# Performance work log

Hardware: AMD Instinct MI355X
Metric: run time of the kernel (lower is better)

## Reference

```python
import jax, jax.numpy as jnp
import numpy as np

DECAY_EPS = 1e-8  # matches F.cosine_similarity eps
DECAY_RATE = 0.999  # buffer decay_rate


def setup_inputs() -> dict:
    key = jax.random.key(0)
    ks = jax.random.split(key, 6)
    B, M, D = 256, 65536, 1024
    return {
        "query": jax.random.normal(ks[0], (B, D), dtype=jnp.float32),
        "mem_keys": jax.random.normal(ks[1], (M, D), dtype=jnp.float32),
        "mem_values": jax.random.normal(ks[2], (M, D), dtype=jnp.float32),
        "importance": jax.random.uniform(ks[3], (M,), dtype=jnp.float32),
        "access_times": jax.random.randint(ks[4], (M,), 0, 1000, dtype=jnp.int32),
        "access_counts": jax.random.randint(ks[5], (M,), 1, 50, dtype=jnp.int32),
        "current_time": 1000,
        "top_k": 8,
    }


def reference(query, mem_keys, mem_values, importance, access_times, access_counts, current_time, top_k):
    # Batched version of AdaptiveMemoryBuffer.retrieve.
    # query: [B, D]; mem_keys/mem_values: [M, D]; importance/access_*: [M]
    qn = query / jnp.maximum(jnp.linalg.norm(query, axis=-1, keepdims=True), DECAY_EPS)
    kn = mem_keys / jnp.maximum(jnp.linalg.norm(mem_keys, axis=-1, keepdims=True), DECAY_EPS)
    sim = qn @ kn.T  # [B, M] cosine similarity

    dt = (current_time - access_times).astype(jnp.float32)           # time since access
    retention = jnp.power(jnp.float32(DECAY_RATE), dt)               # forgetting curve
    freq_bonus = jnp.log1p(access_counts.astype(jnp.float32))        # log(1 + count)
    scores = sim * (retention * importance * freq_bonus)[None, :]    # [B, M]

    top_scores, top_idx = jax.lax.top_k(scores, top_k)                # [B, k]
    weights = jax.nn.softmax(top_scores, axis=-1)                     # [B, k]
    combined = jnp.einsum('bk,bkd->bd', weights, mem_values[top_idx]) # weighted gather
    confidence = weights.max(axis=-1)                                 # [B]
    return combined, confidence
```

## Files before the change

kernel.cpp:

```cpp
#include <hip/hip_runtime.h>
#include <math.h>
#include <float.h>

typedef __attribute__((ext_vector_type(8))) short short8;
typedef __attribute__((ext_vector_type(8))) ushort ushort8;
typedef __attribute__((ext_vector_type(4))) float f32x4;

namespace {

constexpr int B = 256;
constexpr int M = 65536;
constexpr int D = 1024;
constexpr float DECAY_EPS = 1e-8f;
constexpr float DECAY_RATE = 0.999f;

constexpr int BN = 64;
constexpr int BK = 32;
constexpr int KSTEPS = D / BK;

constexpr int CHUNKS = 8;
constexpr int CHUNK = M / CHUNKS;
constexpr int NCAND = CHUNKS * 8;

__device__ inline ushort f2bf(float f) {
  union { float f; unsigned u; } v; v.f = f;
  unsigned r = v.u + 0x7fffu + ((v.u >> 16) & 1u);
  return (ushort)(r >> 16);
}

__device__ inline float dot4(float4 a) {
  return a.x * a.x + a.y * a.y + a.z * a.z + a.w * a.w;
}

__global__ void prep_q_kernel(const float* __restrict__ q, ushort* __restrict__ qnf) {
  const int r = blockIdx.x;
  const int t = threadIdx.x;
  float4 v = reinterpret_cast<const float4*>(q + (size_t)r * D)[t];
  float ss = dot4(v);
#pragma unroll
  for (int off = 32; off; off >>= 1) ss += __shfl_down(ss, off, 64);
  __shared__ float red[4];
  if ((t & 63) == 0) red[t >> 6] = ss;
  __syncthreads();
  const float inv = 1.0f / fmaxf(sqrtf(red[0] + red[1] + red[2] + red[3]), DECAY_EPS);
  ushort4 o;
  o.x = f2bf(v.x * inv); o.y = f2bf(v.y * inv);
  o.z = f2bf(v.z * inv); o.w = f2bf(v.w * inv);
  const int k0 = t * 4;
  const int kt = k0 >> 5;
  const int lane_slot = (r & 15) + 16 * ((k0 & 31) >> 3);
  const int j0 = k0 & 7;
  *reinterpret_cast<ushort4*>(qnf + (size_t)(kt * 16 + (r >> 4)) * 512 + lane_slot * 8 + j0) = o;
}

__global__ __launch_bounds__(256) void score_gemm_kernel(
    const ushort* __restrict__ qnf, const float* __restrict__ keys,
    const float* __restrict__ importance, const int* __restrict__ atimes,
    const int* __restrict__ acnts, const int* __restrict__ ctime,
    ushort* __restrict__ scores) {
  __shared__ alignas(16) ushort Bs[2][BN * BK];
  __shared__ float cscale[BN];

  const int t = threadIdx.x;
  const int lane = t & 63;
  const int w = t >> 6;
  const int jb = blockIdx.x * BN;

  const int rw = t >> 2;
  const int cw = t & 3;
  const float* kptr = keys + (size_t)(jb + rw) * D + cw * 8;
  const int woff = rw * BK + ((cw ^ ((rw >> 1) & 3)) * 8);

  f32x4 acc[4][4];
#pragma unroll
  for (int f = 0; f < 4; ++f)
#pragma unroll
    for (int n = 0; n < 4; ++n) acc[f][n] = (f32x4)(0.0f);

  float kn2 = 0.0f;

  {
    float4 v0 = *reinterpret_cast<const float4*>(kptr);
    float4 v1 = *reinterpret_cast<const float4*>(kptr + 4);
    kn2 += dot4(v0) + dot4(v1);
    short8 pk;
    pk[0] = (short)f2bf(v0.x); pk[1] = (short)f2bf(v0.y);
    pk[2] = (short)f2bf(v0.z); pk[3] = (short)f2bf(v0.w);
    pk[4] = (short)f2bf(v1.x); pk[5] = (short)f2bf(v1.y);
    pk[6] = (short)f2bf(v1.z); pk[7] = (short)f2bf(v1.w);
    *reinterpret_cast<short8*>(&Bs[0][woff]) = pk;
  }
  __syncthreads();

  int roff[4];
#pragma unroll
  for (int nf = 0; nf < 4; ++nf) {
    const int row = nf * 16 + (lane & 15);
    roff[nf] = row * BK + (((lane >> 4) ^ ((row >> 1) & 3)) * 8);
  }

  for (int kt = 0; kt < KSTEPS; ++kt) {
    const int cur = kt & 1;
    float4 nv0, nv1;
    if (kt + 1 < KSTEPS) {
      nv0 = *reinterpret_cast<const float4*>(kptr + (kt + 1) * BK);
      nv1 = *reinterpret_cast<const float4*>(kptr + (kt + 1) * BK + 4);
    }
    short8 a[4];
    const short8* ap = reinterpret_cast<const short8*>(qnf) + (size_t)(kt * 16 + w * 4) * 64 + lane;
#pragma unroll
    for (int f = 0; f < 4; ++f) a[f] = ap[f * 64];
    short8 bb[4];
#pragma unroll
    for (int nf = 0; nf < 4; ++nf)
      bb[nf] = *reinterpret_cast<const short8*>(&Bs[cur][roff[nf]]);
#pragma unroll
    for (int f = 0; f < 4; ++f)
#pragma unroll
      for (int nf = 0; nf < 4; ++nf)
        acc[f][nf] = __builtin_amdgcn_mfma_f32_16x16x32_bf16(a[f], bb[nf], acc[f][nf], 0, 0, 0);
    if (kt + 1 < KSTEPS) {
      kn2 += dot4(nv0) + dot4(nv1);
      short8 pk;
      pk[0] = (short)f2bf(nv0.x); pk[1] = (short)f2bf(nv0.y);
      pk[2] = (short)f2bf(nv0.z); pk[3] = (short)f2bf(nv0.w);
      pk[4] = (short)f2bf(nv1.x); pk[5] = (short)f2bf(nv1.y);
      pk[6] = (short)f2bf(nv1.z); pk[7] = (short)f2bf(nv1.w);
      *reinterpret_cast<short8*>(&Bs[cur ^ 1][woff]) = pk;
    }
    __syncthreads();
  }

  kn2 += __shfl_xor(kn2, 1, 64);
  kn2 += __shfl_xor(kn2, 2, 64);
  if (cw == 0) {
    const int j = jb + rw;
    const float dt = (float)(ctime[0] - atimes[j]);
    const float mult = powf(DECAY_RATE, dt) * importance[j] * log1pf((float)acnts[j]);
    cscale[rw] = mult / fmaxf(sqrtf(kn2), DECAY_EPS);
  }
  __syncthreads();

  const int q = lane & 15;
  float cs[4];
#pragma unroll
  for (int nf = 0; nf < 4; ++nf) cs[nf] = cscale[nf * 16 + q];
#pragma unroll
  for (int f = 0; f < 4; ++f) {
    const int row0 = (w * 4 + f) * 16 + ((lane >> 4) << 2);
#pragma unroll
    for (int nf = 0; nf < 4; ++nf) {
#pragma unroll
      for (int rr = 0; rr < 4; ++rr) {
        const float v = acc[f][nf][rr] * cs[nf];
        const float vn = __shfl_xor(v, 1, 64);
        if (!(q & 1)) {
          const uint pk = (uint)f2bf(v) | ((uint)f2bf(vn) << 16);
          *reinterpret_cast<uint*>(
              scores + (size_t)(row0 + rr) * M + jb + nf * 16 + q) = pk;
        }
      }
    }
  }
}

__global__ __launch_bounds__(256) void topk_partial_kernel(
    const ushort* __restrict__ scores, int* __restrict__ cand_i) {
  const int b = blockIdx.y;
  const int c = blockIdx.x;
  const int t = threadIdx.x;
  const int lane = t & 63, w = t >> 6;
  const ushort8* base8 =
      reinterpret_cast<const ushort8*>(scores + (size_t)b * M + (size_t)c * CHUNK);

  uint s8[8];
#pragma unroll
  for (int i = 0; i < 8; ++i) s8[i] = 0;

  auto ins = [&](uint x) {
    if (x > s8[0]) {
#pragma unroll
      for (int i = 0; i < 8; ++i) {
        const bool up = (i < 7) && (x > s8[i + 1]);
        const uint keep = (x > s8[i]) ? x : s8[i];
        s8[i] = up ? s8[i + 1] : keep;
      }
    }
  };

  const uint jbase = (uint)c * CHUNK;
#pragma unroll
  for (int it = 0; it < CHUNK / (256 * 8); ++it) {
    const int slot = it * 256 + t;
    const ushort8 v = base8[slot];
    const uint j0 = jbase + (uint)slot * 8;
#pragma unroll
    for (int e = 0; e < 8; ++e) {
      const ushort s = (ushort)v[e];
      const ushort key = (s & 0x8000) ? (ushort)~s : (ushort)(s | 0x8000);
      ins(((uint)key << 16) | ((j0 + e) & 0xFFFFu));
    }
  }

  __shared__ uint ls[2048];
#pragma unroll
  for (int i = 0; i < 8; ++i) ls[t * 8 + i] = s8[i];
  __syncthreads();

  __shared__ uint rs4[4];
  __shared__ int rp4[4];
  for (int r = 0; r < 8; ++r) {
    uint ms = 0;
    int mp = 0;
#pragma unroll
    for (int i = 0; i < 8; ++i) {
      const uint v = ls[i * 256 + t];
      if (v > ms) { ms = v; mp = i * 256 + t; }
    }
#pragma unroll
    for (int off = 32; off; off >>= 1) {
      const uint ov = __shfl_xor(ms, off, 64);
      const int op = __shfl_xor(mp, off, 64);
      if (ov > ms) { ms = ov; mp = op; }
    }
    if (lane == 0) { rs4[w] = ms; rp4[w] = mp; }
    __syncthreads();
    if (t == 0) {
      uint bs = 0;
      int bp = 0;
#pragma unroll
      for (int i = 0; i < 4; ++i)
        if (rs4[i] > bs) { bs = rs4[i]; bp = rp4[i]; }
      cand_i[((size_t)b * CHUNKS + c) * 8 + r] = (int)(ls[bp] & 0xFFFFu);
      ls[bp] = 0;
    }
    __syncthreads();
  }
}

__global__ __launch_bounds__(512) void rescore_kernel(
    const int* __restrict__ cand_i, const float* __restrict__ query,
    const float* __restrict__ keys, const float* __restrict__ values,
    const float* __restrict__ importance, const int* __restrict__ atimes,
    const int* __restrict__ acnts, const int* __restrict__ ctime,
    float* __restrict__ outc, float* __restrict__ conf) {
  const int b = blockIdx.x;
  const int t = threadIdx.x;
  const int lane = t & 63, w = t >> 6;

  const float4* qv4 = reinterpret_cast<const float4*>(query + (size_t)b * D + lane * 16);
  float4 q0 = qv4[0], q1 = qv4[1], q2 = qv4[2], q3 = qv4[3];
  float ssq = dot4(q0) + dot4(q1) + dot4(q2) + dot4(q3);
#pragma unroll
  for (int off = 32; off; off >>= 1) ssq += __shfl_xor(ssq, off, 64);
  const float qdn = fmaxf(sqrtf(ssq), DECAY_EPS);
  const int ct = ctime[0];

  __shared__ float sc[NCAND];
  __shared__ int sidx[NCAND];

  for (int u = 0; u < 8; ++u) {
    const int c = w * 8 + u;
    const int j = cand_i[(size_t)b * NCAND + c];
    const float4* kv4 = reinterpret_cast<const float4*>(keys + (size_t)j * D + lane * 16);
    const float4 k0 = kv4[0], k1 = kv4[1], k2 = kv4[2], k3 = kv4[3];
    float dd = q0.x * k0.x + q0.y * k0.y + q0.z * k0.z + q0.w * k0.w
             + q1.x * k1.x + q1.y * k1.y + q1.z * k1.z + q1.w * k1.w
             + q2.x * k2.x + q2.y * k2.y + q2.z * k2.z + q2.w * k2.w
             + q3.x * k3.x + q3.y * k3.y + q3.z * k3.z + q3.w * k3.w;
    float nn = dot4(k0) + dot4(k1) + dot4(k2) + dot4(k3);
#pragma unroll
    for (int off = 32; off; off >>= 1) {
      dd += __shfl_xor(dd, off, 64);
      nn += __shfl_xor(nn, off, 64);
    }
    if (lane == 0) {
      const float dtv = (float)(ct - atimes[j]);
      const float mult = powf(DECAY_RATE, dtv) * importance[j] * log1pf((float)acnts[j]);
      sc[c] = dd / (qdn * fmaxf(sqrtf(nn), DECAY_EPS)) * mult;
      sidx[c] = j;
    }
  }
  __syncthreads();

  __shared__ float w8s[8];
  __shared__ int g8[8];
  __shared__ float confv;
  __shared__ float tls[8];
  __shared__ int tli[8];
  if (w == 0) {
    float myv = sc[lane];
    for (int r = 0; r < 8; ++r) {
      float m = myv;
      int mi = lane;
#pragma unroll
      for (int off = 32; off; off >>= 1) {
        const float ov = __shfl_xor(m, off, 64);
        const int oi = __shfl_xor(mi, off, 64);
        if (ov > m || (ov == m && oi < mi)) { m = ov; mi = oi; }
      }
      if (lane == 0) { tls[r] = m; tli[r] = mi; }
      if (lane == mi) myv = -FLT_MAX;
    }
    if (lane == 0) {
      const float mx = tls[0];
      float e[8];
      float z = 0.0f;
#pragma unroll
      for (int r = 0; r < 8; ++r) { e[r] = expf(tls[r] - mx); z += e[r]; }
      const float invz = 1.0f / z;
#pragma unroll
      for (int r = 0; r < 8; ++r) { w8s[r] = e[r] * invz; g8[r] = sidx[tli[r]]; }
      confv = w8s[0];
    }
  }
  __syncthreads();

  float2 acc = make_float2(0.0f, 0.0f);
#pragma unroll
  for (int k = 0; k < 8; ++k) {
    const float wk = w8s[k];
    const float2 v = *reinterpret_cast<const float2*>(values + (size_t)g8[k] * D + 2 * t);
    acc.x = fmaf(wk, v.x, acc.x);
    acc.y = fmaf(wk, v.y, acc.y);
  }
  *reinterpret_cast<float2*>(outc + (size_t)b * D + 2 * t) = acc;
  if (t == 0) conf[b] = confv;
}

}

extern "C" void kernel_launch(void* const* d_in, const int* in_sizes, int n_in,
                              void* d_out, int out_size, void* d_ws, size_t ws_size,
                              hipStream_t stream) {
  const float* query = (const float*)d_in[0];
  const float* keys = (const float*)d_in[1];
  const float* values = (const float*)d_in[2];
  const float* importance = (const float*)d_in[3];
  const int* atimes = (const int*)d_in[4];
  const int* acnts = (const int*)d_in[5];
  const int* ctime = (const int*)d_in[6];

  float* out = (float*)d_out;
  ushort* qnf = (ushort*)d_ws;
  ushort* scores = qnf + (size_t)B * D;
  int* cand = (int*)(scores + (size_t)B * M);

  prep_q_kernel<<<B, 256, 0, stream>>>(query, qnf);
  score_gemm_kernel<<<M / BN, 256, 0, stream>>>(qnf, keys, importance, atimes,
                                                acnts, ctime, scores);
  dim3 gA(CHUNKS, B);
  topk_partial_kernel<<<gA, 256, 0, stream>>>(scores, cand);
  rescore_kernel<<<B, 512, 0, stream>>>(cand, query, keys, values, importance,
                                        atimes, acnts, ctime, out, out + (size_t)B * D);
}
```

Before: 156.1 us.

## Pre-normalize keys into MFMA-ready bf16 layout in a separate pass

Adds a prep_k kernel that normalizes each key row, folds in the retention/importance/frequency scale, and writes the result as bf16 in the exact fragment layout the MFMA consumes. The score GEMM then loads A and B fragments straight from global memory with register double-buffering, with no LDS staging, no barriers and no epilogue scaling. The trade is an extra pass that reads the 256MB fp32 keys and writes a 128MB bf16 copy, then rereads that copy, in exchange for a simpler, sync-free GEMM loop. Scaling before bf16 rounding also changes rounding slightly.

```diff
diff --git a/kernel.cpp b/kernel.cpp
--- a/kernel.cpp
+++ b/kernel.cpp
@@ -15,8 +15,8 @@
 constexpr float DECAY_RATE = 0.999f;
 
 constexpr int BN = 64;
-constexpr int BK = 32;
-constexpr int KSTEPS = D / BK;
+constexpr int KSTEPS = D / 32;
+constexpr int NT = M / 16;
 
 constexpr int CHUNKS = 8;
 constexpr int CHUNK = M / CHUNKS;
@@ -53,23 +53,62 @@
   *reinterpret_cast<ushort4*>(qnf + (size_t)(kt * 16 + (r >> 4)) * 512 + lane_slot * 8 + j0) = o;
 }
 
+__global__ __launch_bounds__(256) void prep_k_kernel(
+    const float* __restrict__ keys, const float* __restrict__ importance,
+    const int* __restrict__ atimes, const int* __restrict__ acnts,
+    const int* __restrict__ ctime, ushort* __restrict__ knf) {
+  const int jb = blockIdx.x * 16;
+  const int t = threadIdx.x;
+  const int rl = t >> 4;
+  const int c = t & 15;
+  const int j = jb + rl;
+  const float* kp = keys + (size_t)j * D;
+
+  float4 v[16];
+  float ss = 0.0f;
+#pragma unroll
+  for (int i = 0; i < 8; ++i) {
+    const int o = c + 16 * i;
+    v[2 * i] = *reinterpret_cast<const float4*>(kp + o * 8);
+    v[2 * i + 1] = *reinterpret_cast<const float4*>(kp + o * 8 + 4);
+    ss += dot4(v[2 * i]) + dot4(v[2 * i + 1]);
+  }
+  ss += __shfl_xor(ss, 1, 64);
+  ss += __shfl_xor(ss, 2, 64);
+  ss += __shfl_xor(ss, 4, 64);
+  ss += __shfl_xor(ss, 8, 64);
+
+  const float dt = (float)(ctime[0] - atimes[j]);
+  const float mult = powf(DECAY_RATE, dt) * importance[j] * log1pf((float)acnts[j]);
+  const float scale = mult / fmaxf(sqrtf(ss), DECAY_EPS);
+
+  const int nt = j >> 4, q = j & 15;
+#pragma unroll
+  for (int i = 0; i < 8; ++i) {
+    const int o = c + 16 * i;
+    const int kt = o >> 2, h = o & 3;
+    const float4 u0 = v[2 * i], u1 = v[2 * i + 1];
+    short8 pk;
+    pk[0] = (short)f2bf(u0.x * scale); pk[1] = (short)f2bf(u0.y * scale);
+    pk[2] = (short)f2bf(u0.z * scale); pk[3] = (short)f2bf(u0.w * scale);
+    pk[4] = (short)f2bf(u1.x * scale); pk[5] = (short)f2bf(u1.y * scale);
+    pk[6] = (short)f2bf(u1.z * scale); pk[7] = (short)f2bf(u1.w * scale);
+    *reinterpret_cast<short8*>(
+        knf + ((size_t)(kt * NT + nt) * 64 + h * 16 + q) * 8) = pk;
+  }
+}
+
 __global__ __launch_bounds__(256) void score_gemm_kernel(
-    const ushort* __restrict__ qnf, const float* __restrict__ keys,
-    const float* __restrict__ importance, const int* __restrict__ atimes,
-    const int* __restrict__ acnts, const int* __restrict__ ctime,
+    const ushort* __restrict__ qnf, const ushort* __restrict__ knf,
     ushort* __restrict__ scores) {
-  __shared__ alignas(16) ushort Bs[2][BN * BK];
-  __shared__ float cscale[BN];
-
   const int t = threadIdx.x;
   const int lane = t & 63;
   const int w = t >> 6;
-  const int jb = blockIdx.x * BN;
-
-  const int rw = t >> 2;
-  const int cw = t & 3;
-  const float* kptr = keys + (size_t)(jb + rw) * D + cw * 8;
-  const int woff = rw * BK + ((cw ^ ((rw >> 1) & 3)) * 8);
+  const int nt0 = blockIdx.x * 4;
+  const int jb = nt0 * 16;
+
+  const short8* ab = reinterpret_cast<const short8*>(qnf) + (size_t)(w * 4) * 64 + lane;
+  const short8* bb = reinterpret_cast<const short8*>(knf) + (size_t)nt0 * 64 + lane;
 
   f32x4 acc[4][4];
 #pragma unroll
@@ -77,74 +116,33 @@
 #pragma unroll
     for (int n = 0; n < 4; ++n) acc[f][n] = (f32x4)(0.0f);
 
-  float kn2 = 0.0f;
-
-  {
-    float4 v0 = *reinterpret_cast<const float4*>(kptr);
-    float4 v1 = *reinterpret_cast<const float4*>(kptr + 4);
-    kn2 += dot4(v0) + dot4(v1);
-    short8 pk;
-    pk[0] = (short)f2bf(v0.x); pk[1] = (short)f2bf(v0.y);
-    pk[2] = (short)f2bf(v0.z); pk[3] = (short)f2bf(v0.w);
-    pk[4] = (short)f2bf(v1.x); pk[5] = (short)f2bf(v1.y);
-    pk[6] = (short)f2bf(v1.z); pk[7] = (short)f2bf(v1.w);
-    *reinterpret_cast<short8*>(&Bs[0][woff]) = pk;
-  }
-  __syncthreads();
-
-  int roff[4];
-#pragma unroll
-  for (int nf = 0; nf < 4; ++nf) {
-    const int row = nf * 16 + (lane & 15);
-    roff[nf] = row * BK + (((lane >> 4) ^ ((row >> 1) & 3)) * 8);
-  }
-
-  for (int kt = 0; kt < KSTEPS; ++kt) {
-    const int cur = kt & 1;
-    float4 nv0, nv1;
-    if (kt + 1 < KSTEPS) {
-      nv0 = *reinterpret_cast<const float4*>(kptr + (kt + 1) * BK);
-      nv1 = *reinterpret_cast<const float4*>(kptr + (kt + 1) * BK + 4);
-    }
-    short8 a[4];
-    const short8* ap = reinterpret_cast<const short8*>(qnf) + (size_t)(kt * 16 + w * 4) * 64 + lane;
-#pragma unroll
-    for (int f = 0; f < 4; ++f) a[f] = ap[f * 64];
-    short8 bb[4];
-#pragma unroll
-    for (int nf = 0; nf < 4; ++nf)
-      bb[nf] = *reinterpret_cast<const short8*>(&Bs[cur][roff[nf]]);
+  short8 aA[4], bA[4], aB[4], bB[4];
+
+  auto LA = [&](short8* a, int s) {
+#pragma unroll
+    for (int f = 0; f < 4; ++f) a[f] = ab[(size_t)(s * 16 + f) * 64];
+  };
+  auto LB = [&](short8* b, int s) {
+#pragma unroll
+    for (int nf = 0; nf < 4; ++nf) b[nf] = bb[((size_t)s * NT + nf) * 64];
+  };
+  auto CMP = [&](short8* a, short8* b) {
 #pragma unroll
     for (int f = 0; f < 4; ++f)
 #pragma unroll
       for (int nf = 0; nf < 4; ++nf)
-        acc[f][nf] = __builtin_amdgcn_mfma_f32_16x16x32_bf16(a[f], bb[nf], acc[f][nf], 0, 0, 0);
-    if (kt + 1 < KSTEPS) {
-      kn2 += dot4(nv0) + dot4(nv1);
-      short8 pk;
-      pk[0] = (short)f2bf(nv0.x); pk[1] = (short)f2bf(nv0.y);
-      pk[2] = (short)f2bf(nv0.z); pk[3] = (short)f2bf(nv0.w);
-      pk[4] = (short)f2bf(nv1.x); pk[5] = (short)f2bf(nv1.y);
-      pk[6] = (short)f2bf(nv1.z); pk[7] = (short)f2bf(nv1.w);
-      *reinterpret_cast<short8*>(&Bs[cur ^ 1][woff]) = pk;
-    }
-    __syncthreads();
-  }
-
-  kn2 += __shfl_xor(kn2, 1, 64);
-  kn2 += __shfl_xor(kn2, 2, 64);
-  if (cw == 0) {
-    const int j = jb + rw;
-    const float dt = (float)(ctime[0] - atimes[j]);
-    const float mult = powf(DECAY_RATE, dt) * importance[j] * log1pf((float)acnts[j]);
-    cscale[rw] = mult / fmaxf(sqrtf(kn2), DECAY_EPS);
-  }
-  __syncthreads();
+        acc[f][nf] = __builtin_amdgcn_mfma_f32_16x16x32_bf16(a[f], b[nf], acc[f][nf], 0, 0, 0);
+  };
+
+  LA(aA, 0); LB(bA, 0);
+  for (int it = 0; it < KSTEPS / 2; ++it) {
+    LA(aB, 2 * it + 1); LB(bB, 2 * it + 1);
+    CMP(aA, bA);
+    if (it < KSTEPS / 2 - 1) { LA(aA, 2 * it + 2); LB(bA, 2 * it + 2); }
+    CMP(aB, bB);
+  }
 
   const int q = lane & 15;
-  float cs[4];
-#pragma unroll
-  for (int nf = 0; nf < 4; ++nf) cs[nf] = cscale[nf * 16 + q];
 #pragma unroll
   for (int f = 0; f < 4; ++f) {
     const int row0 = (w * 4 + f) * 16 + ((lane >> 4) << 2);
@@ -152,7 +150,7 @@
     for (int nf = 0; nf < 4; ++nf) {
 #pragma unroll
       for (int rr = 0; rr < 4; ++rr) {
-        const float v = acc[f][nf][rr] * cs[nf];
+        const float v = acc[f][nf][rr];
         const float vn = __shfl_xor(v, 1, 64);
         if (!(q & 1)) {
           const uint pk = (uint)f2bf(v) | ((uint)f2bf(vn) << 16);
@@ -342,13 +340,16 @@
   const int* ctime = (const int*)d_in[6];
 
   float* out = (float*)d_out;
-  ushort* qnf = (ushort*)d_ws;
-  ushort* scores = qnf + (size_t)B * D;
-  int* cand = (int*)(scores + (size_t)B * M);
+  char* ws = (char*)d_ws;
+  ushort* qnf = (ushort*)ws;
+  ushort* scores = (ushort*)(ws + (1 << 19));
+  int* cand = (int*)(ws + (1 << 19) + ((size_t)B * M * 2));
+  ushort* knf = (ushort*)(ws + (1 << 19) + ((size_t)B * M * 2) + (1 << 16));
 
   prep_q_kernel<<<B, 256, 0, stream>>>(query, qnf);
-  score_gemm_kernel<<<M / BN, 256, 0, stream>>>(qnf, keys, importance, atimes,
-                                                acnts, ctime, scores);
+  prep_k_kernel<<<M / 16, 256, 0, stream>>>(keys, importance, atimes, acnts,
+                                            ctime, knf);
+  score_gemm_kernel<<<M / BN, 256, 0, stream>>>(qnf, knf, scores);
   dim3 gA(CHUNKS, B);
   topk_partial_kernel<<<gA, 256, 0, stream>>>(scores, cand);
   rescore_kernel<<<B, 512, 0, stream>>>(cand, query, keys, values, importance,
```

New measurement: 190.7 us. +22.2%, slower.

## Retile score GEMM to 128x128 blocks with direct global-to-LDS async loads

Applied to the files above, without the earlier changes.

The score GEMM now uses 128x128 output tiles over a 2D grid that also splits the query batch. Query and fp32 key tiles are streamed straight into shared memory with global_load_lds using swizzled source addresses, and the bf16 conversion and key-norm accumulation happen when fragments are read from LDS. The normalized query is stored row-major instead of in a pre-swizzled fragment layout. The aim is to overlap global loads with MFMA work and cut register staging, but each key tile is now fetched by two blocks, which may double HBM traffic on the dominant stream unless the cache absorbs it.

```diff
diff --git a/kernel.cpp b/kernel.cpp
--- a/kernel.cpp
+++ b/kernel.cpp
@@ -5,6 +5,9 @@
 typedef __attribute__((ext_vector_type(8))) short short8;
 typedef __attribute__((ext_vector_type(8))) ushort ushort8;
 typedef __attribute__((ext_vector_type(4))) float f32x4;
+
+#define AS1 __attribute__((address_space(1)))
+#define AS3 __attribute__((address_space(3)))
 
 namespace {
 
@@ -14,8 +17,7 @@
 constexpr float DECAY_EPS = 1e-8f;
 constexpr float DECAY_RATE = 0.999f;
 
-constexpr int BN = 64;
-constexpr int BK = 32;
+constexpr int BM = 128, BN = 128, BK = 32;
 constexpr int KSTEPS = D / BK;
 
 constexpr int CHUNKS = 8;
@@ -26,6 +28,15 @@
   union { float f; unsigned u; } v; v.f = f;
   unsigned r = v.u + 0x7fffu + ((v.u >> 16) & 1u);
   return (ushort)(r >> 16);
+}
+
+__device__ inline short8 pack8(float4 u, float4 v) {
+  short8 r;
+  r[0] = (short)f2bf(u.x); r[1] = (short)f2bf(u.y);
+  r[2] = (short)f2bf(u.z); r[3] = (short)f2bf(u.w);
+  r[4] = (short)f2bf(v.x); r[5] = (short)f2bf(v.y);
+  r[6] = (short)f2bf(v.z); r[7] = (short)f2bf(v.w);
+  return r;
 }
 
 __device__ inline float dot4(float4 a) {
@@ -46,11 +57,7 @@
   ushort4 o;
   o.x = f2bf(v.x * inv); o.y = f2bf(v.y * inv);
   o.z = f2bf(v.z * inv); o.w = f2bf(v.w * inv);
-  const int k0 = t * 4;
-  const int kt = k0 >> 5;
-  const int lane_slot = (r & 15) + 16 * ((k0 & 31) >> 3);
-  const int j0 = k0 & 7;
-  *reinterpret_cast<ushort4*>(qnf + (size_t)(kt * 16 + (r >> 4)) * 512 + lane_slot * 8 + j0) = o;
+  *reinterpret_cast<ushort4*>(qnf + (size_t)r * D + t * 4) = o;
 }
 
 __global__ __launch_bounds__(256) void score_gemm_kernel(
@@ -58,106 +65,112 @@
     const float* __restrict__ importance, const int* __restrict__ atimes,
     const int* __restrict__ acnts, const int* __restrict__ ctime,
     ushort* __restrict__ scores) {
-  __shared__ alignas(16) ushort Bs[2][BN * BK];
-  __shared__ float cscale[BN];
+  __shared__ alignas(16) ushort Al[2][BM * BK];
+  __shared__ alignas(16) float Bl[2][BN * BK];
 
   const int t = threadIdx.x;
   const int lane = t & 63;
   const int w = t >> 6;
+  const int wm = w >> 1;
+  const int wn = w & 1;
+  const int q = lane & 15;
+  const int h = lane >> 4;
   const int jb = blockIdx.x * BN;
-
-  const int rw = t >> 2;
-  const int cw = t & 3;
-  const float* kptr = keys + (size_t)(jb + rw) * D + cw * 8;
-  const int woff = rw * BK + ((cw ^ ((rw >> 1) & 3)) * 8);
+  const int ib = blockIdx.y * BM;
+
+  const int ar = t >> 2, asl = t & 3;
+  const ushort* ag = qnf + (size_t)(ib + ar) * D + (asl ^ (ar & 3)) * 8;
+  const int br = t >> 3, bsl = t & 7;
+  const float* bg = keys + (size_t)(jb + br) * D + (bsl ^ (br & 7)) * 4;
+
+  int aoff[4];
+#pragma unroll
+  for (int f = 0; f < 4; ++f)
+    aoff[f] = ((wm * 4 + f) * 16 + q) * BK + ((h ^ (q & 3)) * 8);
+  int boff0[4], boff1[4];
+#pragma unroll
+  for (int n = 0; n < 4; ++n) {
+    const int r = (wn * 4 + n) * 16 + q;
+    boff0[n] = r * BK + (((2 * h) ^ (q & 7)) * 4);
+    boff1[n] = r * BK + (((2 * h + 1) ^ (q & 7)) * 4);
+  }
 
   f32x4 acc[4][4];
 #pragma unroll
   for (int f = 0; f < 4; ++f)
 #pragma unroll
     for (int n = 0; n < 4; ++n) acc[f][n] = (f32x4)(0.0f);
-
-  float kn2 = 0.0f;
-
-  {
-    float4 v0 = *reinterpret_cast<const float4*>(kptr);
-    float4 v1 = *reinterpret_cast<const float4*>(kptr + 4);
-    kn2 += dot4(v0) + dot4(v1);
-    short8 pk;
-    pk[0] = (short)f2bf(v0.x); pk[1] = (short)f2bf(v0.y);
-    pk[2] = (short)f2bf(v0.z); pk[3] = (short)f2bf(v0.w);
-    pk[4] = (short)f2bf(v1.x); pk[5] = (short)f2bf(v1.y);
-    pk[6] = (short)f2bf(v1.z); pk[7] = (short)f2bf(v1.w);
-    *reinterpret_cast<short8*>(&Bs[0][woff]) = pk;
-  }
-  __syncthreads();
-
-  int roff[4];
-#pragma unroll
-  for (int nf = 0; nf < 4; ++nf) {
-    const int row = nf * 16 + (lane & 15);
-    roff[nf] = row * BK + (((lane >> 4) ^ ((row >> 1) & 3)) * 8);
-  }
-
-  for (int kt = 0; kt < KSTEPS; ++kt) {
-    const int cur = kt & 1;
-    float4 nv0, nv1;
-    if (kt + 1 < KSTEPS) {
-      nv0 = *reinterpret_cast<const float4*>(kptr + (kt + 1) * BK);
-      nv1 = *reinterpret_cast<const float4*>(kptr + (kt + 1) * BK + 4);
-    }
-    short8 a[4];
-    const short8* ap = reinterpret_cast<const short8*>(qnf) + (size_t)(kt * 16 + w * 4) * 64 + lane;
-#pragma unroll
-    for (int f = 0; f < 4; ++f) a[f] = ap[f * 64];
-    short8 bb[4];
-#pragma unroll
-    for (int nf = 0; nf < 4; ++nf)
-      bb[nf] = *reinterpret_cast<const short8*>(&Bs[cur][roff[nf]]);
+  float kn[4] = {0.0f, 0.0f, 0.0f, 0.0f};
+
+  auto stage = [&](int s, int buf) {
+    const ushort* a0 = ag + s * BK;
+    __builtin_amdgcn_global_load_lds((const AS1 void*)a0,
+                                     (AS3 void*)(&Al[buf][w * 512]), 16, 0, 0);
+    __builtin_amdgcn_global_load_lds((const AS1 void*)(a0 + (size_t)64 * D),
+                                     (AS3 void*)(&Al[buf][2048 + w * 512]), 16, 0, 0);
+    const float* b0 = bg + s * BK;
+#pragma unroll
+    for (int i = 0; i < 4; ++i)
+      __builtin_amdgcn_global_load_lds((const AS1 void*)(b0 + (size_t)(i * 32) * D),
+                                       (AS3 void*)(&Bl[buf][i * 1024 + w * 256]), 16, 0, 0);
+  };
+
+  stage(0, 0);
+  __syncthreads();
+
+  for (int s = 0; s < KSTEPS; ++s) {
+    const int cur = s & 1;
+    if (s + 1 < KSTEPS) stage(s + 1, cur ^ 1);
+
+    short8 af[4];
 #pragma unroll
     for (int f = 0; f < 4; ++f)
-#pragma unroll
-      for (int nf = 0; nf < 4; ++nf)
-        acc[f][nf] = __builtin_amdgcn_mfma_f32_16x16x32_bf16(a[f], bb[nf], acc[f][nf], 0, 0, 0);
-    if (kt + 1 < KSTEPS) {
-      kn2 += dot4(nv0) + dot4(nv1);
-      short8 pk;
-      pk[0] = (short)f2bf(nv0.x); pk[1] = (short)f2bf(nv0.y);
-      pk[2] = (short)f2bf(nv0.z); pk[3] = (short)f2bf(nv0.w);
-      pk[4] = (short)f2bf(nv1.x); pk[5] = (short)f2bf(nv1.y);
-      pk[6] = (short)f2bf(nv1.z); pk[7] = (short)f2bf(nv1.w);
-      *reinterpret_cast<short8*>(&Bs[cur ^ 1][woff]) = pk;
-    }
+      af[f] = *reinterpret_cast<const short8*>(&Al[cur][aoff[f]]);
+    short8 bf[4];
+#pragma unroll
+    for (int n = 0; n < 4; ++n) {
+      const float4 x = *reinterpret_cast<const float4*>(&Bl[cur][boff0[n]]);
+      const float4 y = *reinterpret_cast<const float4*>(&Bl[cur][boff1[n]]);
+      kn[n] += dot4(x) + dot4(y);
+      bf[n] = pack8(x, y);
+    }
+#pragma unroll
+    for (int f = 0; f < 4; ++f)
+#pragma unroll
+      for (int n = 0; n < 4; ++n)
+        acc[f][n] = __builtin_amdgcn_mfma_f32_16x16x32_bf16(af[f], bf[n], acc[f][n], 0, 0, 0);
+
     __syncthreads();
   }
 
-  kn2 += __shfl_xor(kn2, 1, 64);
-  kn2 += __shfl_xor(kn2, 2, 64);
-  if (cw == 0) {
-    const int j = jb + rw;
-    const float dt = (float)(ctime[0] - atimes[j]);
-    const float mult = powf(DECAY_RATE, dt) * importance[j] * log1pf((float)acnts[j]);
-    cscale[rw] = mult / fmaxf(sqrtf(kn2), DECAY_EPS);
-  }
-  __syncthreads();
-
-  const int q = lane & 15;
+#pragma unroll
+  for (int n = 0; n < 4; ++n) {
+    kn[n] += __shfl_xor(kn[n], 16, 64);
+    kn[n] += __shfl_xor(kn[n], 32, 64);
+  }
+  const int ct = ctime[0];
   float cs[4];
 #pragma unroll
-  for (int nf = 0; nf < 4; ++nf) cs[nf] = cscale[nf * 16 + q];
+  for (int n = 0; n < 4; ++n) {
+    const int j = jb + (wn * 4 + n) * 16 + q;
+    const float mult = powf(DECAY_RATE, (float)(ct - atimes[j])) * importance[j] *
+                       log1pf((float)acnts[j]);
+    cs[n] = mult / fmaxf(sqrtf(kn[n]), DECAY_EPS);
+  }
+
 #pragma unroll
   for (int f = 0; f < 4; ++f) {
-    const int row0 = (w * 4 + f) * 16 + ((lane >> 4) << 2);
-#pragma unroll
-    for (int nf = 0; nf < 4; ++nf) {
+    const int row0 = ib + (wm * 4 + f) * 16 + (h << 2);
+#pragma unroll
+    for (int n = 0; n < 4; ++n) {
+      const int col = jb + (wn * 4 + n) * 16 + q;
 #pragma unroll
       for (int rr = 0; rr < 4; ++rr) {
-        const float v = acc[f][nf][rr] * cs[nf];
+        const float v = acc[f][n][rr] * cs[n];
         const float vn = __shfl_xor(v, 1, 64);
         if (!(q & 1)) {
           const uint pk = (uint)f2bf(v) | ((uint)f2bf(vn) << 16);
-          *reinterpret_cast<uint*>(
-              scores + (size_t)(row0 + rr) * M + jb + nf * 16 + q) = pk;
+          *reinterpret_cast<uint*>(scores + (size_t)(row0 + rr) * M + col) = pk;
         }
       }
     }
@@ -347,8 +360,9 @@
   int* cand = (int*)(scores + (size_t)B * M);
 
   prep_q_kernel<<<B, 256, 0, stream>>>(query, qnf);
-  score_gemm_kernel<<<M / BN, 256, 0, stream>>>(qnf, keys, importance, atimes,
-                                                acnts, ctime, scores);
+  dim3 gG(M / BN, B / BM);
+  score_gemm_kernel<<<gG, 256, 0, stream>>>(qnf, keys, importance, atimes,
+                                            acnts, ctime, scores);
   dim3 gA(CHUNKS, B);
   topk_partial_kernel<<<gA, 256, 0, stream>>>(scores, cand);
   rescore_kernel<<<B, 512, 0, stream>>>(cand, query, keys, values, importance,
```

Result: slower. 205.1 us (+31.4%).
